# Performance work log

Measured on AMD Instinct MI355X. Metric: run time of the kernel, lower is better.

Reference implementation:

```python
import jax, jax.numpy as jnp
import numpy as np

D = 768  # hidden dim hard-coded in the module


def setup_inputs() -> dict:
    key = jax.random.key(0)
    k1, k2, k3, k4, k5 = jax.random.split(key, 5)
    N, M = 512, 512
    return {
        "text_output": jax.random.normal(k1, (N, D), dtype=jnp.float32),
        "visual_output": jax.random.normal(k2, (M, D), dtype=jnp.float32),
        "W1": jax.random.normal(k3, (D, D), dtype=jnp.float32),
        "W2": jax.random.normal(k4, (D, D), dtype=jnp.float32),
        "W3": jax.random.normal(k5, (D, D), dtype=jnp.float32),
    }


def reference(text_output, visual_output, W1, W2, W3):
    # C[n,m] = tanh( (text @ W1) . visual[m] )
    C = jnp.tanh((text_output @ W1) @ visual_output.T)            # (N, M)
    W2_text = text_output @ W2                                    # (N, D)
    W3_visual = visual_output @ W3.T                              # (M, D)
    # M[n,m,:] = tanh(W2_text[n] + W3_visual[m] * C[n,m])
    Mt = jnp.tanh(W2_text[:, None, :] + W3_visual[None, :, :] * C[..., None])  # (N, M, D)
    # score[n,m] = text[n] . M[n,m]  (replaces the per-row Python loop)
    score = jnp.einsum("nd,nmd->nm", text_output, Mt)             # (N, M)
    return score
```

## Files before the change

### kernel.cpp

```cpp
#include <hip/hip_runtime.h>

#define DD   768
#define NN   512
#define MM   512

#define PRE_K 2.88539008177792681472f

typedef _Float16 h8 __attribute__((ext_vector_type(8)));
typedef __attribute__((ext_vector_type(4))) float f32x4;

__device__ __forceinline__ float fexp(float x) { return __builtin_amdgcn_exp2f(x); }
__device__ __forceinline__ float frcp(float x) { return __builtin_amdgcn_rcpf(x); }
__device__ __forceinline__ float fast_tanh(float x) {
  return 1.0f - 2.0f * frcp(fexp(PRE_K * x) + 1.0f);
}

__device__ __forceinline__ void splitf(float x, ushort& h, ushort& l) {
  const _Float16 hh = (_Float16)x;
  const _Float16 ll = (_Float16)(x - (float)hh);
  h = __builtin_bit_cast(unsigned short, hh);
  l = __builtin_bit_cast(unsigned short, ll);
}

__global__ __launch_bounds__(256) void prep_kernel(
    const float* __restrict__ text, const float* __restrict__ visual,
    const float* __restrict__ W1, const float* __restrict__ W2,
    const float* __restrict__ W3,
    ushort* __restrict__ th, ushort* __restrict__ tl,
    ushort* __restrict__ vh, ushort* __restrict__ vl,
    ushort* __restrict__ w3h, ushort* __restrict__ w3l,
    ushort* __restrict__ w1th, ushort* __restrict__ w1tl,
    ushort* __restrict__ w2th, ushort* __restrict__ w2tl)
{
  __shared__ float Lt[32][33];
  const int b = blockIdx.x;
  const int t = threadIdx.x;

  if (b < 1344) {
    const float* src; ushort *dh, *dl; size_t off;
    if (b < 384)      { src = text;   dh = th;  dl = tl;  off = (size_t)b * 1024; }
    else if (b < 768) { src = visual; dh = vh;  dl = vl;  off = (size_t)(b - 384) * 1024; }
    else              { src = W3;     dh = w3h; dl = w3l; off = (size_t)(b - 768) * 1024; }
    const size_t i = off + (size_t)t * 4;
    const float4 v = *(const float4*)&src[i];
    ushort4 h, l;
    splitf(v.x, h.x, l.x); splitf(v.y, h.y, l.y);
    splitf(v.z, h.z, l.z); splitf(v.w, h.w, l.w);
    *(ushort4*)&dh[i] = h;
    *(ushort4*)&dl[i] = l;
  } else {
    const int tt = b - 1344;
    const bool second = tt >= 576;
    const int tile = second ? tt - 576 : tt;
    const float* W = second ? W2 : W1;
    ushort* oh = second ? w2th : w1th;
    ushort* ol = second ? w2tl : w1tl;
    const int k0 = (tile / 24) * 32, j0 = (tile % 24) * 32;
    {
      const int k = t >> 3, j4 = (t & 7) * 4;
      const float4 v = *(const float4*)&W[(size_t)(k0 + k) * DD + j0 + j4];
      Lt[j4 + 0][k] = v.x; Lt[j4 + 1][k] = v.y;
      Lt[j4 + 2][k] = v.z; Lt[j4 + 3][k] = v.w;
    }
    __syncthreads();
    {
      const int j = t >> 3, k4 = (t & 7) * 4;
      ushort4 h, l;
      splitf(Lt[j][k4 + 0], h.x, l.x); splitf(Lt[j][k4 + 1], h.y, l.y);
      splitf(Lt[j][k4 + 2], h.z, l.z); splitf(Lt[j][k4 + 3], h.w, l.w);
      *(ushort4*)&oh[(size_t)(j0 + j) * DD + k0 + k4] = h;
      *(ushort4*)&ol[(size_t)(j0 + j) * DD + k0 + k4] = l;
    }
  }
}

#define BK   32
#define LROW 40
#define APL  (32 * LROW)
#define BPL  (64 * LROW)

template <bool ALO>
__device__ __forceinline__ void gemm_core32(
    ushort* __restrict__ As, ushort* __restrict__ Bs,
    const ushort* __restrict__ Ahg, const ushort* __restrict__ Alg,
    const ushort* __restrict__ Bhg, const ushort* __restrict__ Blg,
    int i0, int j0, int nsteps, f32x4* acc)
{
  const int tid = threadIdx.x;
  const int row = tid >> 2;
  const int ks8 = (tid & 3) * 8;
  const bool doA = (row < 32);
  const size_t ga = (size_t)(i0 + row) * DD + ks8;
  const size_t gb = (size_t)(j0 + row) * DD + ks8;
  const int lw = row * LROW + ks8;

  const int lane = tid & 63, wave = tid >> 6;
  const int r15 = lane & 15, quad = lane >> 4;
  const int wr = wave >> 1, wc = wave & 1;
  const int fa = (wr * 16 + r15) * LROW + quad * 8;
  const int fb = (wc * 32 + r15) * LROW + quad * 8;

  h8 pah, pal, pbh, pbl;
  if (doA) {
    pah = *(const h8*)(Ahg + ga);
    if (ALO) pal = *(const h8*)(Alg + ga);
  }
  pbh = *(const h8*)(Bhg + gb);
  pbl = *(const h8*)(Blg + gb);

  int p = 0;
  if (doA) {
    *(h8*)&As[lw] = pah;
    if (ALO) *(h8*)&As[APL + lw] = pal;
  }
  *(h8*)&Bs[lw] = pbh;
  *(h8*)&Bs[BPL + lw] = pbl;
  __syncthreads();

  for (int s = 0; s < nsteps; ++s) {
    const bool more = (s + 1 < nsteps);
    if (more) {
      if (doA) {
        pah = *(const h8*)(Ahg + ga + (s + 1) * BK);
        if (ALO) pal = *(const h8*)(Alg + ga + (s + 1) * BK);
      }
      pbh = *(const h8*)(Bhg + gb + (s + 1) * BK);
      pbl = *(const h8*)(Blg + gb + (s + 1) * BK);
    }
    ushort* Ac = As + p * 2 * APL;
    ushort* Bc = Bs + p * 2 * BPL;
    const h8 a_h = *(const h8*)&Ac[fa];
    h8 a_l; if (ALO) a_l = *(const h8*)&Ac[APL + fa];
    h8 b_h[2], b_l[2];
    #pragma unroll
    for (int c = 0; c < 2; ++c) {
      b_h[c] = *(const h8*)&Bc[fb + c * 16 * LROW];
      b_l[c] = *(const h8*)&Bc[BPL + fb + c * 16 * LROW];
    }
    #pragma unroll
    for (int c = 0; c < 2; ++c)
      acc[c] = __builtin_amdgcn_mfma_f32_16x16x32_f16(a_h, b_h[c], acc[c], 0, 0, 0);
    #pragma unroll
    for (int c = 0; c < 2; ++c)
      acc[c] = __builtin_amdgcn_mfma_f32_16x16x32_f16(a_h, b_l[c], acc[c], 0, 0, 0);
    if (ALO) {
      #pragma unroll
      for (int c = 0; c < 2; ++c)
        acc[c] = __builtin_amdgcn_mfma_f32_16x16x32_f16(a_l, b_h[c], acc[c], 0, 0, 0);
    }
    if (more) {
      const int q = p ^ 1;
      ushort* An = As + q * 2 * APL;
      ushort* Bn = Bs + q * 2 * BPL;
      if (doA) {
        *(h8*)&An[lw] = pah;
        if (ALO) *(h8*)&An[APL + lw] = pal;
      }
      *(h8*)&Bn[lw] = pbh;
      *(h8*)&Bn[BPL + lw] = pbl;
    }
    __syncthreads();
    p ^= 1;
  }
}

__global__ __launch_bounds__(256) void mfma1_kernel(
    const ushort* __restrict__ th, const ushort* __restrict__ tl,
    const ushort* __restrict__ vh, const ushort* __restrict__ vl,
    const ushort* __restrict__ w1th, const ushort* __restrict__ w1tl,
    const ushort* __restrict__ w2th, const ushort* __restrict__ w2tl,
    const ushort* __restrict__ w3h, const ushort* __restrict__ w3l,
    ushort* __restrict__ Ah, ushort* __restrict__ Al,
    float* __restrict__ kw2t, float* __restrict__ kw3v)
{
  __shared__ ushort As[2 * 2 * APL];
  __shared__ ushort Bs[2 * 2 * BPL];

  const int z  = blockIdx.z;
  const int j0 = blockIdx.x * 64;
  const int i0 = blockIdx.y * 32;

  f32x4 acc[2];
  acc[0] = (f32x4){0.f, 0.f, 0.f, 0.f};
  acc[1] = (f32x4){0.f, 0.f, 0.f, 0.f};

  if (z == 0)
    gemm_core32<true >(As, Bs, th, tl, w1th, w1tl, i0, j0, DD / BK, acc);
  else if (z == 1)
    gemm_core32<false>(As, Bs, th, tl, w2th, w2tl, i0, j0, DD / BK, acc);
  else
    gemm_core32<false>(As, Bs, vh, vl, w3h,  w3l,  i0, j0, DD / BK, acc);

  const int lane = threadIdx.x & 63, wave = threadIdx.x >> 6;
  const int r15 = lane & 15, quad = lane >> 4;
  const int wr = wave >> 1, wc = wave & 1;
  if (z == 0) {
    #pragma unroll
    for (int c = 0; c < 2; ++c)
      #pragma unroll
      for (int r = 0; r < 4; ++r) {
        const size_t o = (size_t)(i0 + wr * 16 + quad * 4 + r) * DD
                       + j0 + wc * 32 + c * 16 + r15;
        splitf(acc[c][r], Ah[o], Al[o]);
      }
  } else {
    float* Out = (z == 1) ? kw2t : kw3v;
    #pragma unroll
    for (int c = 0; c < 2; ++c)
      #pragma unroll
      for (int r = 0; r < 4; ++r)
        Out[(size_t)(i0 + wr * 16 + quad * 4 + r) * DD + j0 + wc * 32 + c * 16 + r15] =
            acc[c][r] * PRE_K;
  }
}

#define DCH  64
#define MLDW 68
#define NCH  (DD / DCH)

__global__ __launch_bounds__(256) void main_kernel(
    const float* __restrict__ text, const float* __restrict__ kw2t,
    const float* __restrict__ kw3v,
    const ushort* __restrict__ Ah, const ushort* __restrict__ Al,
    const ushort* __restrict__ vh, const ushort* __restrict__ vl,
    float* __restrict__ out)
{
  __shared__ float sbuf[2][64 * MLDW];

  const int tid = threadIdx.x;
  const int nl = tid >> 4;
  const int ml = tid & 15;
  const int n0 = blockIdx.y * 16;
  const int m0 = blockIdx.x * 32;
  const int lane = tid & 63, wave = tid >> 6;
  const int r15 = lane & 15, quad = lane >> 4;

  const size_t aoff  = (size_t)(n0 + r15) * DD + wave * (DD / 4) + quad * 8;
  const size_t b0off = (size_t)(m0 + r15) * DD + wave * (DD / 4) + quad * 8;
  const size_t b1off = (size_t)(m0 + 16 + r15) * DD + wave * (DD / 4) + quad * 8;
  const ushort* Ap  = Ah + aoff;
  const ushort* Alp = Al + aoff;
  const ushort* B0h = vh + b0off;
  const ushort* B0l = vl + b0off;
  const ushort* B1h = vh + b1off;
  const ushort* B1l = vl + b1off;

  f32x4 q0 = {0.f, 0.f, 0.f, 0.f}, q1 = {0.f, 0.f, 0.f, 0.f};
  h8 cah  = *(const h8*)Ap;
  h8 cal  = *(const h8*)Alp;
  h8 cb0h = *(const h8*)B0h;
  h8 cb0l = *(const h8*)B0l;
  h8 cb1h = *(const h8*)B1h;
  h8 cb1l = *(const h8*)B1l;
  #pragma unroll
  for (int s = 0; s < (DD / 4) / BK; ++s) {
    h8 nah, nal, nb0h, nb0l, nb1h, nb1l;
    const bool more = (s + 1 < (DD / 4) / BK);
    if (more) {
      nah  = *(const h8*)(Ap  + (s + 1) * BK);
      nal  = *(const h8*)(Alp + (s + 1) * BK);
      nb0h = *(const h8*)(B0h + (s + 1) * BK);
      nb0l = *(const h8*)(B0l + (s + 1) * BK);
      nb1h = *(const h8*)(B1h + (s + 1) * BK);
      nb1l = *(const h8*)(B1l + (s + 1) * BK);
    }
    q0 = __builtin_amdgcn_mfma_f32_16x16x32_f16(cah, cb0h, q0, 0, 0, 0);
    q1 = __builtin_amdgcn_mfma_f32_16x16x32_f16(cah, cb1h, q1, 0, 0, 0);
    q0 = __builtin_amdgcn_mfma_f32_16x16x32_f16(cah, cb0l, q0, 0, 0, 0);
    q1 = __builtin_amdgcn_mfma_f32_16x16x32_f16(cah, cb1l, q1, 0, 0, 0);
    q0 = __builtin_amdgcn_mfma_f32_16x16x32_f16(cal, cb0h, q0, 0, 0, 0);
    q1 = __builtin_amdgcn_mfma_f32_16x16x32_f16(cal, cb1h, q1, 0, 0, 0);
    if (more) { cah = nah; cal = nal; cb0h = nb0h; cb0l = nb0l; cb1h = nb1h; cb1l = nb1l; }
  }

  float (*Qs)[16][32] = (float (*)[16][32])(&sbuf[0][0]);
  #pragma unroll
  for (int r = 0; r < 4; ++r) {
    Qs[wave][quad * 4 + r][r15]      = q0[r];
    Qs[wave][quad * 4 + r][16 + r15] = q1[r];
  }
  __syncthreads();
  float sA = Qs[0][nl][ml];
  sA += Qs[1][nl][ml]; sA += Qs[2][nl][ml]; sA += Qs[3][nl][ml];
  float sB = Qs[0][nl][ml + 16];
  sB += Qs[1][nl][ml + 16]; sB += Qs[2][nl][ml + 16]; sB += Qs[3][nl][ml + 16];
  const float cA = fast_tanh(sA);
  const float cB = fast_tanh(sB);
  __syncthreads();

  const int n  = n0 + nl;
  const int mA = m0 + ml, mB = mA + 16;

  float4 aA = {0.f, 0.f, 0.f, 0.f};
  float4 aB = {0.f, 0.f, 0.f, 0.f};
  float4 ts = {0.f, 0.f, 0.f, 0.f};

  const int srow = tid >> 4;
  const int sc4  = (tid & 15) << 2;
  const float* gt  = &text[(size_t)(n0 + srow) * DD + sc4];
  const float* g2  = &kw2t[(size_t)(n0 + srow) * DD + sc4];
  const float* g3a = &kw3v[(size_t)(m0 + srow) * DD + sc4];
  const float* g3b = &kw3v[(size_t)(m0 + 16 + srow) * DD + sc4];
  const int wt  = srow * MLDW + sc4;
  const int w2  = (16 + srow) * MLDW + sc4;
  const int w3a = (32 + srow) * MLDW + sc4;
  const int w3b = (48 + srow) * MLDW + sc4;

  float4 rt  = *(const float4*)gt;
  float4 r2  = *(const float4*)g2;
  float4 r3a = *(const float4*)g3a;
  float4 r3b = *(const float4*)g3b;
  int p = 0;
  *(float4*)&sbuf[0][wt]  = rt;
  *(float4*)&sbuf[0][w2]  = r2;
  *(float4*)&sbuf[0][w3a] = r3a;
  *(float4*)&sbuf[0][w3b] = r3b;
  __syncthreads();

  #pragma unroll 4
  for (int c = 0; c < NCH; ++c) {
    const bool more = (c + 1 < NCH);
    if (more) {
      rt  = *(const float4*)(gt  + (c + 1) * DCH);
      r2  = *(const float4*)(g2  + (c + 1) * DCH);
      r3a = *(const float4*)(g3a + (c + 1) * DCH);
      r3b = *(const float4*)(g3b + (c + 1) * DCH);
    }
    const float* bp = sbuf[p];
    #pragma unroll 4
    for (int j = 0; j < DCH; j += 4) {
      const float4 tv  = *(const float4*)&bp[nl * MLDW + j];
      const float4 w2v = *(const float4*)&bp[(16 + nl) * MLDW + j];
      const float4 w3A = *(const float4*)&bp[(32 + ml) * MLDW + j];
      const float4 w3B = *(const float4*)&bp[(48 + ml) * MLDW + j];
      ts.x += tv.x; ts.y += tv.y; ts.z += tv.z; ts.w += tv.w;
      aA.x = fmaf(tv.x, frcp(fexp(fmaf(w3A.x, cA, w2v.x)) + 1.0f), aA.x);
      aA.y = fmaf(tv.y, frcp(fexp(fmaf(w3A.y, cA, w2v.y)) + 1.0f), aA.y);
      aA.z = fmaf(tv.z, frcp(fexp(fmaf(w3A.z, cA, w2v.z)) + 1.0f), aA.z);
      aA.w = fmaf(tv.w, frcp(fexp(fmaf(w3A.w, cA, w2v.w)) + 1.0f), aA.w);
      aB.x = fmaf(tv.x, frcp(fexp(fmaf(w3B.x, cB, w2v.x)) + 1.0f), aB.x);
      aB.y = fmaf(tv.y, frcp(fexp(fmaf(w3B.y, cB, w2v.y)) + 1.0f), aB.y);
      aB.z = fmaf(tv.z, frcp(fexp(fmaf(w3B.z, cB, w2v.z)) + 1.0f), aB.z);
      aB.w = fmaf(tv.w, frcp(fexp(fmaf(w3B.w, cB, w2v.w)) + 1.0f), aB.w);
    }
    if (more) {
      const int q = p ^ 1;
      *(float4*)&sbuf[q][wt]  = rt;
      *(float4*)&sbuf[q][w2]  = r2;
      *(float4*)&sbuf[q][w3a] = r3a;
      *(float4*)&sbuf[q][w3b] = r3b;
    }
    __syncthreads();
    p ^= 1;
  }

  const float tsum = (ts.x + ts.y) + (ts.z + ts.w);
  float* op = out + (size_t)n * MM;
  op[mA] = fmaf(-2.0f, (aA.x + aA.y) + (aA.z + aA.w), tsum);
  op[mB] = fmaf(-2.0f, (aB.x + aB.y) + (aB.z + aB.w), tsum);
}

extern "C" void kernel_launch(void* const* d_in, const int* in_sizes, int n_in,
                              void* d_out, int out_size, void* d_ws, size_t ws_size,
                              hipStream_t stream) {
  const float* text   = (const float*)d_in[0];
  const float* visual = (const float*)d_in[1];
  const float* W1     = (const float*)d_in[2];
  const float* W2     = (const float*)d_in[3];
  const float* W3     = (const float*)d_in[4];
  float* out = (float*)d_out;

  char* base = (char*)d_ws;
  ushort* th   = (ushort*)(base);
  ushort* tl   = (ushort*)(base + 786432);
  ushort* vh   = (ushort*)(base + 1572864);
  ushort* vl   = (ushort*)(base + 2359296);
  ushort* w1th = (ushort*)(base + 3145728);
  ushort* w1tl = (ushort*)(base + 4325376);
  ushort* w2th = (ushort*)(base + 5505024);
  ushort* w2tl = (ushort*)(base + 6684672);
  ushort* w3h  = (ushort*)(base + 7864320);
  ushort* w3l  = (ushort*)(base + 9043968);
  ushort* Ah   = (ushort*)(base + 10223616);
  ushort* Al   = (ushort*)(base + 11010048);
  float*  kw2t = (float*) (base + 11796480);
  float*  kw3v = (float*) (base + 13369344);

  hipLaunchKernelGGL(prep_kernel, dim3(2496), dim3(256), 0, stream,
                     text, visual, W1, W2, W3,
                     th, tl, vh, vl, w3h, w3l, w1th, w1tl, w2th, w2tl);
  hipLaunchKernelGGL(mfma1_kernel, dim3(DD / 64, NN / 32, 3), dim3(256), 0, stream,
                     th, tl, vh, vl, w1th, w1tl, w2th, w2tl, w3h, w3l,
                     Ah, Al, kw2t, kw3v);
  hipLaunchKernelGGL(main_kernel, dim3(MM / 32, NN / 16), dim3(256), 0, stream,
                     text, kw2t, kw3v, Ah, Al, vh, vl, out);
}
```

Baseline: 136.2 us.

## Split main kernel over D into three slices with atomic accumulation

Adds a third grid dimension to the main kernel so each block handles a 256-wide slice of the hidden dimension. Partial scores are combined with float atomic adds. The output is pre-seeded with the per-row text sum by extra blocks in the prep kernel. The text and kw2t rows are now read directly from global memory (broadcast within the row) rather than staged in shared memory, which shrinks LDS use and raises the number of blocks, to improve occupancy and parallelism. In exchange, each block recomputes the C-score MFMA prologue three times, and atomics make the summation order nondeterministic.

After: 142.3 us. 1.05x slower.

```diff
diff --git a/kernel.cpp b/kernel.cpp
--- a/kernel.cpp
+++ b/kernel.cpp
@@ -30,7 +30,8 @@
     ushort* __restrict__ vh, ushort* __restrict__ vl,
     ushort* __restrict__ w3h, ushort* __restrict__ w3l,
     ushort* __restrict__ w1th, ushort* __restrict__ w1tl,
-    ushort* __restrict__ w2th, ushort* __restrict__ w2tl)
+    ushort* __restrict__ w2th, ushort* __restrict__ w2tl,
+    float* __restrict__ out)
 {
   __shared__ float Lt[32][33];
   const int b = blockIdx.x;
@@ -48,7 +49,7 @@
     splitf(v.z, h.z, l.z); splitf(v.w, h.w, l.w);
     *(ushort4*)&dh[i] = h;
     *(ushort4*)&dl[i] = l;
-  } else {
+  } else if (b < 2496) {
     const int tt = b - 1344;
     const bool second = tt >= 576;
     const int tile = second ? tt - 576 : tt;
@@ -71,6 +72,27 @@
       *(ushort4*)&oh[(size_t)(j0 + j) * DD + k0 + k4] = h;
       *(ushort4*)&ol[(size_t)(j0 + j) * DD + k0 + k4] = l;
     }
+  } else {
+    float* red = (float*)Lt;
+    const int u = b - 2496;
+    const int n0 = u * 2;
+    const int half = t >> 7;
+    const int lt = t & 127;
+
+    const float* tr = text + (size_t)(n0 + half) * DD;
+    float s = 0.f;
+    #pragma unroll
+    for (int i = 0; i < DD / 128; ++i) s += tr[lt + i * 128];
+    red[t] = s;
+    __syncthreads();
+    #pragma unroll
+    for (int st = 64; st > 0; st >>= 1) {
+      if (lt < st) red[t] += red[t + st];
+      __syncthreads();
+    }
+    const float Tn = red[half << 7];
+    float4 o; o.x = Tn; o.y = Tn; o.z = Tn; o.w = Tn;
+    *(float4*)&out[(size_t)(n0 + half) * MM + lt * 4] = o;
   }
 }
 
@@ -214,9 +236,9 @@
   }
 }
 
-#define DCH  64
-#define MLDW 68
-#define NCH  (DD / DCH)
+#define DCH    64
+#define DRANGE 256
+#define MLDW   68
 
 __global__ __launch_bounds__(256) void main_kernel(
     const float* __restrict__ text, const float* __restrict__ kw2t,
@@ -225,13 +247,14 @@
     const ushort* __restrict__ vh, const ushort* __restrict__ vl,
     float* __restrict__ out)
 {
-  __shared__ float sbuf[2][64 * MLDW];
+  __shared__ float sbuf[2][32 * MLDW];
 
   const int tid = threadIdx.x;
   const int nl = tid >> 4;
   const int ml = tid & 15;
   const int n0 = blockIdx.y * 16;
   const int m0 = blockIdx.x * 32;
+  const int z  = blockIdx.z;
   const int lane = tid & 63, wave = tid >> 6;
   const int r15 = lane & 15, quad = lane >> 4;
 
@@ -273,7 +296,7 @@
     if (more) { cah = nah; cal = nal; cb0h = nb0h; cb0l = nb0l; cb1h = nb1h; cb1l = nb1l; }
   }
 
-  float (*Qs)[16][32] = (float (*)[16][32])(&sbuf[0][0]);
+  float (*Qs)[16][33] = (float (*)[16][33])(&sbuf[0][0]);
   #pragma unroll
   for (int r = 0; r < 4; ++r) {
     Qs[wave][quad * 4 + r][r15]      = q0[r];
@@ -290,50 +313,44 @@
 
   const int n  = n0 + nl;
   const int mA = m0 + ml, mB = mA + 16;
+  const int dbase = z * DRANGE;
 
   float4 aA = {0.f, 0.f, 0.f, 0.f};
   float4 aB = {0.f, 0.f, 0.f, 0.f};
-  float4 ts = {0.f, 0.f, 0.f, 0.f};
+
+  const float* gt = &text[(size_t)n * DD + dbase];
+  const float* g2 = &kw2t[(size_t)n * DD + dbase];
 
   const int srow = tid >> 4;
   const int sc4  = (tid & 15) << 2;
-  const float* gt  = &text[(size_t)(n0 + srow) * DD + sc4];
-  const float* g2  = &kw2t[(size_t)(n0 + srow) * DD + sc4];
-  const float* g3a = &kw3v[(size_t)(m0 + srow) * DD + sc4];
-  const float* g3b = &kw3v[(size_t)(m0 + 16 + srow) * DD + sc4];
-  const int wt  = srow * MLDW + sc4;
-  const int w2  = (16 + srow) * MLDW + sc4;
-  const int w3a = (32 + srow) * MLDW + sc4;
-  const int w3b = (48 + srow) * MLDW + sc4;
-
-  float4 rt  = *(const float4*)gt;
-  float4 r2  = *(const float4*)g2;
+  const float* g3a = &kw3v[(size_t)(m0 + srow) * DD + dbase + sc4];
+  const float* g3b = &kw3v[(size_t)(m0 + 16 + srow) * DD + dbase + sc4];
+  const int w3a = srow * MLDW + sc4;
+  const int w3b = (16 + srow) * MLDW + sc4;
+
   float4 r3a = *(const float4*)g3a;
   float4 r3b = *(const float4*)g3b;
   int p = 0;
-  *(float4*)&sbuf[0][wt]  = rt;
-  *(float4*)&sbuf[0][w2]  = r2;
   *(float4*)&sbuf[0][w3a] = r3a;
   *(float4*)&sbuf[0][w3b] = r3b;
   __syncthreads();
 
-  #pragma unroll 4
-  for (int c = 0; c < NCH; ++c) {
-    const bool more = (c + 1 < NCH);
+  #pragma unroll
+  for (int c = 0; c < DRANGE / DCH; ++c) {
+    const bool more = (c + 1 < DRANGE / DCH);
     if (more) {
-      rt  = *(const float4*)(gt  + (c + 1) * DCH);
-      r2  = *(const float4*)(g2  + (c + 1) * DCH);
       r3a = *(const float4*)(g3a + (c + 1) * DCH);
       r3b = *(const float4*)(g3b + (c + 1) * DCH);
     }
     const float* bp = sbuf[p];
+    const float* gtc = gt + c * DCH;
+    const float* g2c = g2 + c * DCH;
     #pragma unroll 4
     for (int j = 0; j < DCH; j += 4) {
-      const float4 tv  = *(const float4*)&bp[nl * MLDW + j];
-      const float4 w2v = *(const float4*)&bp[(16 + nl) * MLDW + j];
-      const float4 w3A = *(const float4*)&bp[(32 + ml) * MLDW + j];
-      const float4 w3B = *(const float4*)&bp[(48 + ml) * MLDW + j];
-      ts.x += tv.x; ts.y += tv.y; ts.z += tv.z; ts.w += tv.w;
+      const float4 tv  = *(const float4*)&gtc[j];
+      const float4 w2v = *(const float4*)&g2c[j];
+      const float4 w3A = *(const float4*)&bp[ml * MLDW + j];
+      const float4 w3B = *(const float4*)&bp[(16 + ml) * MLDW + j];
       aA.x = fmaf(tv.x, frcp(fexp(fmaf(w3A.x, cA, w2v.x)) + 1.0f), aA.x);
       aA.y = fmaf(tv.y, frcp(fexp(fmaf(w3A.y, cA, w2v.y)) + 1.0f), aA.y);
       aA.z = fmaf(tv.z, frcp(fexp(fmaf(w3A.z, cA, w2v.z)) + 1.0f), aA.z);
@@ -345,8 +362,6 @@
     }
     if (more) {
       const int q = p ^ 1;
-      *(float4*)&sbuf[q][wt]  = rt;
-      *(float4*)&sbuf[q][w2]  = r2;
       *(float4*)&sbuf[q][w3a] = r3a;
       *(float4*)&sbuf[q][w3b] = r3b;
     }
@@ -354,10 +369,9 @@
     p ^= 1;
   }
 
-  const float tsum = (ts.x + ts.y) + (ts.z + ts.w);
   float* op = out + (size_t)n * MM;
-  op[mA] = fmaf(-2.0f, (aA.x + aA.y) + (aA.z + aA.w), tsum);
-  op[mB] = fmaf(-2.0f, (aB.x + aB.y) + (aB.z + aB.w), tsum);
+  unsafeAtomicAdd(&op[mA], -2.0f * ((aA.x + aA.y) + (aA.z + aA.w)));
+  unsafeAtomicAdd(&op[mB], -2.0f * ((aB.x + aB.y) + (aB.z + aB.w)));
 }
 
 extern "C" void kernel_launch(void* const* d_in, const int* in_sizes, int n_in,
@@ -386,12 +400,12 @@
   float*  kw2t = (float*) (base + 11796480);
   float*  kw3v = (float*) (base + 13369344);
 
-  hipLaunchKernelGGL(prep_kernel, dim3(2496), dim3(256), 0, stream,
+  hipLaunchKernelGGL(prep_kernel, dim3(2752), dim3(256), 0, stream,
                      text, visual, W1, W2, W3,
-                     th, tl, vh, vl, w3h, w3l, w1th, w1tl, w2th, w2tl);
+                     th, tl, vh, vl, w3h, w3l, w1th, w1tl, w2th, w2tl, out);
   hipLaunchKernelGGL(mfma1_kernel, dim3(DD / 64, NN / 32, 3), dim3(256), 0, stream,
                      th, tl, vh, vl, w1th, w1tl, w2th, w2tl, w3h, w3l,
                      Ah, Al, kw2t, kw3v);
-  hipLaunchKernelGGL(main_kernel, dim3(MM / 32, NN / 16), dim3(256), 0, stream,
+  hipLaunchKernelGGL(main_kernel, dim3(MM / 32, NN / 16, 3), dim3(256), 0, stream,
                      text, kw2t, kw3v, Ah, Al, vh, vl, out);
 }
```
